# Kernel tuning notes

Measured on AMD Instinct MI355X. Metric: run time of the kernel, lower is better.

## Reference

```python
import jax, jax.numpy as jnp
import numpy as np

B, N, FIN, FOUT, H = 8, 2048, 128, 128, 2


def setup_inputs() -> dict:
    key = jax.random.key(0)
    k_h, k_adj, k_w, k_a = jax.random.split(key, 4)
    h = jax.random.normal(k_h, (B, N, FIN), dtype=jnp.float32)
    adj = jax.random.randint(k_adj, (B, N, N), 0, 2).astype(jnp.int32)
    # self-loops so no softmax row is all -inf
    idx = jnp.arange(N)
    adj = adj.at[:, idx, idx].set(1)
    W = jax.random.normal(k_w, (H, FIN, FOUT), dtype=jnp.float32) * 0.1
    a = jax.random.normal(k_a, (H, 2 * FOUT), dtype=jnp.float32) * 0.1
    return {"h": h, "adj": adj, "W": W, "a": a}


def reference(h, adj, W, a):
    # h: [B,N,FIN], adj: [B,N,N] int, W: [H,FIN,FOUT], a: [H,2*FOUT]
    Fout = W.shape[-1]
    Wh = jnp.einsum('bnf,hfo->bhno', h, W)              # [B,H,N,FOUT]
    # decompose a^T [Wh_i || Wh_j] = a1.Wh_i + a2.Wh_j (exact same math,
    # avoids the [B,N,N,2F] concat the torch code materializes)
    a1, a2 = a[:, :Fout], a[:, Fout:]
    s_i = jnp.einsum('bhno,ho->bhn', Wh, a1)            # score from node i
    s_j = jnp.einsum('bhno,ho->bhn', Wh, a2)            # score from node j
    e = jax.nn.leaky_relu(s_i[:, :, :, None] + s_j[:, :, None, :], 0.2)  # [B,H,N,N]
    e = jnp.where(adj[:, None, :, :] == 0, -jnp.inf, e)
    att = jax.nn.softmax(e, axis=-1)                    # [B,H,N,N]
    out = jnp.einsum('bhnm,bhmo->bhno', att, Wh)        # [B,H,N,FOUT]
    b, hh, n, f = out.shape
    # concat heads along feature dim (head order matches torch cat)
    return out.transpose(0, 2, 1, 3).reshape(b, n, hh * f)
```

## Files before the change

kernel.cpp:

```cpp
#include <hip/hip_runtime.h>
#include <math.h>

constexpr int Bv   = 8;
constexpr int Nv   = 2048;
constexpr int FIN  = 128;
constexpr int FOUT = 128;
constexpr int NH   = 2;
constexpr float LOG2E = 1.44269504088896340736f;

typedef __attribute__((ext_vector_type(8)))  short short8;
typedef __attribute__((ext_vector_type(4)))  float f32x4;
typedef __attribute__((ext_vector_type(16))) float f32x16;
typedef __attribute__((ext_vector_type(4)))  int   i32x4;
typedef unsigned long long u64;

static __device__ __forceinline__ unsigned short f2bf(float f) {
    unsigned u = __builtin_bit_cast(unsigned, f);
    u += 0x7fffu + ((u >> 16) & 1u);
    return (unsigned short)(u >> 16);
}
static __device__ __forceinline__ float bf2f(unsigned short s) {
    unsigned u = ((unsigned)s) << 16;
    return __builtin_bit_cast(float, u);
}
static __device__ __forceinline__ float fast_exp2(float x) {
#if __has_builtin(__builtin_amdgcn_exp2f)
    return __builtin_amdgcn_exp2f(x);
#else
    return exp2f(x);
#endif
}
static __device__ __forceinline__ unsigned cvt_pk_bf16(float lo, float hi) {
    unsigned r;
    asm("v_cvt_pk_bf16_f32 %0, %1, %2" : "=v"(r) : "v"(lo), "v"(hi));
    return r;
}

__global__ __launch_bounds__(256) void wa_kernel(const float* __restrict__ W,
                                                 const float* __restrict__ a,
                                                 float* __restrict__ wa,
                                                 unsigned short* __restrict__ wthi,
                                                 unsigned short* __restrict__ wtlo) {
    __shared__ unsigned short shi[FIN * 132];
    __shared__ unsigned short slo[FIN * 132];
    int hh = blockIdx.x;
    int t = threadIdx.x;

    const float* Ws = W + (size_t)hh * FIN * FOUT;
    for (int idx = t; idx < FIN * FOUT; idx += 256) {
        int f = idx >> 7, o = idx & 127;
        float wv = Ws[idx];
        unsigned short uh = f2bf(wv);
        shi[o * 132 + f] = uh;
        slo[o * 132 + f] = f2bf(wv - bf2f(uh));
    }

    int f = t >> 1, half = t & 1;
    const float* Wr = Ws + (size_t)f * FOUT + half * 64;
    const float* ar = a + (size_t)hh * 2 * FOUT + half * 64;
    float s1 = 0.f, s2 = 0.f;
    for (int o = 0; o < 64; o += 4) {
        float4 w4 = *(const float4*)&Wr[o];
        s1 += w4.x * ar[o] + w4.y * ar[o + 1] + w4.z * ar[o + 2] + w4.w * ar[o + 3];
        s2 += w4.x * ar[FOUT + o] + w4.y * ar[FOUT + o + 1] + w4.z * ar[FOUT + o + 2] + w4.w * ar[FOUT + o + 3];
    }
    s1 += __shfl_xor(s1, 1, 64);
    s2 += __shfl_xor(s2, 1, 64);
    if (half == 0) {
        wa[(hh * 2 + 0) * FIN + f] = s1 * LOG2E;
        wa[(hh * 2 + 1) * FIN + f] = s2 * LOG2E;
    }

    __syncthreads();
    unsigned short* dhi = wthi + (size_t)hh * FOUT * FIN;
    unsigned short* dlo = wtlo + (size_t)hh * FOUT * FIN;
    for (int idx = t; idx < FIN * FOUT; idx += 256) {
        int o = idx >> 7, ff = idx & 127;
        dhi[idx] = shi[o * 132 + ff];
        dlo[idx] = slo[o * 132 + ff];
    }
}

__global__ __launch_bounds__(256, 4) void prep_kernel(
    const float* __restrict__ h, const int* __restrict__ adj,
    const float* __restrict__ wa,
    const unsigned short* __restrict__ wthi, const unsigned short* __restrict__ wtlo,
    u64* __restrict__ adjp, unsigned short* __restrict__ whf,
    float* __restrict__ si, float* __restrict__ sj) {
    int bid = blockIdx.x;
    int t   = threadIdx.x;

    if (bid < 4096) {
        int wid = bid * 4 + (t >> 6);
        int l   = t & 63;
        int b   = wid >> 11;
        int r5  = wid & 2047;
        int jt  = r5 >> 6;
        int rb  = r5 & 63;
        const int* src = adj + ((size_t)b * Nv + rb * 32) * Nv + jt * 64 + l;
        u64* dst = adjp + ((size_t)b * 32 + jt) * Nv + rb * 32;
        for (int r = 0; r < 32; r += 8) {
            int av[8];
#pragma unroll
            for (int k = 0; k < 8; ++k) av[k] = src[(size_t)(r + k) * Nv];
            u64 m[8];
#pragma unroll
            for (int k = 0; k < 8; ++k) m[k] = __ballot(av[k] != 0);
            if (l == 0) {
#pragma unroll
                for (int k = 0; k < 8; k += 2) {
                    uint4 q = {(unsigned)m[k], (unsigned)(m[k] >> 32),
                               (unsigned)m[k + 1], (unsigned)(m[k + 1] >> 32)};
                    *(uint4*)&dst[r + k] = q;
                }
            }
        }
    } else if (bid < 8192) {
        int row  = (bid - 4096) * 4 + (t >> 6);
        int lane = t & 63;
        float x0 = h[(size_t)row * FIN + lane];
        float x1 = h[(size_t)row * FIN + 64 + lane];
        float s[4];
#pragma unroll
        for (int q = 0; q < 4; ++q) {
            const float* wp = wa + q * FIN;
            s[q] = x0 * wp[lane] + x1 * wp[64 + lane];
        }
#pragma unroll
        for (int m = 32; m >= 1; m >>= 1) {
#pragma unroll
            for (int q = 0; q < 4; ++q) s[q] += __shfl_xor(s[q], m, 64);
        }
        if (lane == 0) {
            int bb = row >> 11, n = row & (Nv - 1);
            si[((size_t)(bb * NH + 0)) * Nv + n] = s[0];
            sj[((size_t)(bb * NH + 0)) * Nv + n] = s[1];
            si[((size_t)(bb * NH + 1)) * Nv + n] = s[2];
            sj[((size_t)(bb * NH + 1)) * Nv + n] = s[3];
        }
    } else {
        int wb2 = bid - 8192;
        int bb  = wb2 & 7;
        int r2  = wb2 >> 3;
        int hh  = r2 & 1;
        int jtb = r2 >> 1;
        int n0  = jtb * 64;

        int w = t >> 6, l = t & 63, lo16 = l & 15, grp = l >> 4;
        int o0 = w * 32;

        const unsigned short* Whi = wthi + (size_t)hh * FOUT * FIN;
        const unsigned short* Wlo = wtlo + (size_t)hh * FOUT * FIN;
        short8 ahi[2][4], alo[2][4];
#pragma unroll
        for (int ot = 0; ot < 2; ++ot)
#pragma unroll
            for (int kt = 0; kt < 4; ++kt) {
                int off = (o0 + ot * 16 + lo16) * FIN + kt * 32 + grp * 8;
                ahi[ot][kt] = *(const short8*)&Whi[off];
                alo[ot][kt] = *(const short8*)&Wlo[off];
            }

        f32x4 acc[2][4];
#pragma unroll
        for (int ot = 0; ot < 2; ++ot)
#pragma unroll
            for (int nt = 0; nt < 4; ++nt) acc[ot][nt] = (f32x4){0.f, 0.f, 0.f, 0.f};

        const float* hb = h + ((size_t)bb * Nv + n0) * FIN;
#pragma unroll
        for (int nt = 0; nt < 4; ++nt) {
#pragma unroll
            for (int kt = 0; kt < 4; ++kt) {
                const float* hp = hb + (size_t)(nt * 16 + lo16) * FIN + kt * 32 + grp * 8;
                float4 x0 = *(const float4*)hp;
                float4 x1 = *(const float4*)(hp + 4);
                float xs[8] = {x0.x, x0.y, x0.z, x0.w, x1.x, x1.y, x1.z, x1.w};
                short8 bhi, blo;
#pragma unroll
                for (int i = 0; i < 8; ++i) {
                    unsigned short uh = f2bf(xs[i]);
                    bhi[i] = (short)uh;
                    blo[i] = (short)f2bf(xs[i] - bf2f(uh));
                }
#pragma unroll
                for (int ot = 0; ot < 2; ++ot) {
                    acc[ot][nt] = __builtin_amdgcn_mfma_f32_16x16x32_bf16(ahi[ot][kt], bhi, acc[ot][nt], 0, 0, 0);
                    acc[ot][nt] = __builtin_amdgcn_mfma_f32_16x16x32_bf16(ahi[ot][kt], blo, acc[ot][nt], 0, 0, 0);
                    acc[ot][nt] = __builtin_amdgcn_mfma_f32_16x16x32_bf16(alo[ot][kt], bhi, acc[ot][nt], 0, 0, 0);
                }
            }
        }
        unsigned short* db = whf + (size_t)(bb * NH + hh) * 262144;
#pragma unroll
        for (int ot = 0; ot < 2; ++ot)
#pragma unroll
            for (int nt = 0; nt < 4; ++nt)
#pragma unroll
                for (int reg = 0; reg < 4; ++reg) {
                    int oc = ot * 16 + grp * 4 + reg;
                    db[(size_t)(((jtb * 4 + nt) * 4 + w) * 64 + (lo16 >> 3) * 32 + oc) * 8 + (lo16 & 7)] =
                        f2bf(acc[ot][nt][reg]);
                }
    }
}

__global__ __launch_bounds__(256, 3) void gat_attn_kernel(
    const u64* __restrict__ adjp, const unsigned short* __restrict__ whf,
    const float* __restrict__ si, const float* __restrict__ sj,
    float* __restrict__ out) {
    int bid = blockIdx.x;
    int bb  = bid & 7;
    int r2  = bid >> 3;
    int rp  = r2 & 31;
    int hh  = (r2 >> 5) & 1;
    int ch  = r2 >> 6;

    int t = threadIdx.x, w = t >> 6, l = t & 63;
    int jp = w & 1, rw = w >> 1;
    int lo32 = l & 31, kh = l >> 5;
    int r0 = rp * 64 + rw * 32;
    int myrow = r0 + lo32;

    float sir = si[(size_t)(bb * NH + hh) * Nv + myrow];
    const u64*   adjr = adjp + (size_t)bb * 32 * Nv + myrow;
    const float* sjb  = sj + (size_t)(bb * NH + hh) * Nv;
    const unsigned short* wbp = whf + (size_t)(bb * NH + hh) * 262144 + (size_t)l * 8;

    f32x16 acc0, acc1, accL;
#pragma unroll
    for (int i = 0; i < 16; ++i) { acc0[i] = 0.f; acc1[i] = 0.f; accL[i] = 0.f; }

    const int ones_w = 0x3f803f80;
    short8 onesf = __builtin_bit_cast(short8, (i32x4){ones_w, ones_w, ones_w, ones_w});

    int jt0 = jp * 16;
    u64 mask = adjr[(size_t)jt0 * Nv];
    for (int jtl = 0; jtl < 16; ++jtl) {
        int jt = jt0 + jtl;
        int jb = jt * 64;
        const unsigned short* fb = wbp + (size_t)(jt * 16 + ch * 2) * 512;
        short8 bf[4][2];
#pragma unroll
        for (int kt = 0; kt < 4; ++kt) {
            bf[kt][0] = *(const short8*)(fb + (kt * 4 + 0) * 512);
            bf[kt][1] = *(const short8*)(fb + (kt * 4 + 1) * 512);
        }
        u64 mcur = mask;
        if (jtl < 15) mask = adjr[(size_t)(jt + 1) * Nv];

        short8 af[4];
#pragma unroll
        for (int kt = 0; kt < 4; ++kt) {
            unsigned mb = (unsigned)(mcur >> (kt * 16 + kh * 8)) & 0xFFu;
            const float* sp = &sjb[jb + kt * 16 + kh * 8];
            float4 s0 = *(const float4*)sp;
            float4 s1 = *(const float4*)(sp + 4);
            float x0 = sir + s0.x, x1 = sir + s0.y, x2 = sir + s0.z, x3 = sir + s0.w;
            float x4 = sir + s1.x, x5 = sir + s1.y, x6 = sir + s1.z, x7 = sir + s1.w;
            x0 = fmaxf(x0, 0.2f * x0); x1 = fmaxf(x1, 0.2f * x1);
            x2 = fmaxf(x2, 0.2f * x2); x3 = fmaxf(x3, 0.2f * x3);
            x4 = fmaxf(x4, 0.2f * x4); x5 = fmaxf(x5, 0.2f * x5);
            x6 = fmaxf(x6, 0.2f * x6); x7 = fmaxf(x7, 0.2f * x7);
            float p0 = fast_exp2(x0), p1 = fast_exp2(x1), p2 = fast_exp2(x2), p3 = fast_exp2(x3);
            float p4 = fast_exp2(x4), p5 = fast_exp2(x5), p6 = fast_exp2(x6), p7 = fast_exp2(x7);
            p0 = (mb & 1u)   ? p0 : 0.f;  p1 = (mb & 2u)   ? p1 : 0.f;
            p2 = (mb & 4u)   ? p2 : 0.f;  p3 = (mb & 8u)   ? p3 : 0.f;
            p4 = (mb & 16u)  ? p4 : 0.f;  p5 = (mb & 32u)  ? p5 : 0.f;
            p6 = (mb & 64u)  ? p6 : 0.f;  p7 = (mb & 128u) ? p7 : 0.f;
            unsigned w0 = cvt_pk_bf16(p0, p1), w1 = cvt_pk_bf16(p2, p3);
            unsigned w2 = cvt_pk_bf16(p4, p5), w3 = cvt_pk_bf16(p6, p7);
            af[kt] = __builtin_bit_cast(short8, (i32x4){(int)w0, (int)w1, (int)w2, (int)w3});
        }
#pragma unroll
        for (int kt = 0; kt < 4; ++kt) {
            acc0 = __builtin_amdgcn_mfma_f32_32x32x16_bf16(af[kt], bf[kt][0], acc0, 0, 0, 0);
            acc1 = __builtin_amdgcn_mfma_f32_32x32x16_bf16(af[kt], bf[kt][1], acc1, 0, 0, 0);
            accL = __builtin_amdgcn_mfma_f32_32x32x16_bf16(af[kt], onesf,    accL, 0, 0, 0);
        }
    }

    __shared__ float red[2][64][49];
    if (jp == 1) {
#pragma unroll
        for (int i = 0; i < 16; ++i) {
            red[rw][l][i]      = acc0[i];
            red[rw][l][16 + i] = acc1[i];
            red[rw][l][32 + i] = accL[i];
        }
    }
    __syncthreads();
    if (jp == 0) {
#pragma unroll
        for (int i = 0; i < 16; ++i) {
            acc0[i] += red[rw][l][i];
            acc1[i] += red[rw][l][16 + i];
            accL[i] += red[rw][l][32 + i];
        }
#pragma unroll
        for (int reg = 0; reg < 16; ++reg) {
            int rowc = (reg & 3) + 8 * (reg >> 2) + 4 * kh;
            float linv = 1.0f / accL[reg];
            float* op = out + ((size_t)(bb * Nv + r0 + rowc)) * (NH * FOUT) + hh * FOUT + ch * 64;
            op[lo32]      = acc0[reg] * linv;
            op[32 + lo32] = acc1[reg] * linv;
        }
    }
}

extern "C" void kernel_launch(void* const* d_in, const int* in_sizes, int n_in,
                              void* d_out, int out_size, void* d_ws, size_t ws_size,
                              hipStream_t stream) {
    const float* h   = (const float*)d_in[0];
    const int*   adj = (const int*)d_in[1];
    const float* W   = (const float*)d_in[2];
    const float* a   = (const float*)d_in[3];
    float*       out = (float*)d_out;

    char* ws = (char*)d_ws;
    unsigned short* whf  = (unsigned short*)ws;
    u64*            adjp = (u64*)(ws + 8388608);
    float* si = (float*)(ws + 8388608 + 4194304);
    float* sj = si + (size_t)Bv * NH * Nv;
    float* wa = sj + (size_t)Bv * NH * Nv;
    unsigned short* wthi = (unsigned short*)(wa + NH * 2 * FIN);
    unsigned short* wtlo = wthi + (size_t)NH * FOUT * FIN;

    wa_kernel  <<<dim3(2),    dim3(256), 0, stream>>>(W, a, wa, wthi, wtlo);
    prep_kernel<<<dim3(8704), dim3(256), 0, stream>>>(h, adj, wa, wthi, wtlo, adjp, whf, si, sj);
    gat_attn_kernel<<<dim3(1024), dim3(256), 0, stream>>>(adjp, whf, si, sj, out);
}
```

Before: 110.6 us.

## Pack adjacency bitmask row-wise with LDS transpose for coalesced stores

The adjacency bit-packing stage is restructured. Each block now handles 64 full rows of one batch, with each wave ballotting 16 rows across all 32 column tiles. The masks are staged in a shared-memory tile and then written to the packed layout with coalesced per-thread stores. This replaces single-lane uint4 stores and strided row reads. The block count drops from 4096 to 256, which may reduce the parallelism available to hide latency while reading the 134MB int adjacency matrix.

```diff
diff --git a/kernel.cpp b/kernel.cpp
--- a/kernel.cpp
+++ b/kernel.cpp
@@ -87,36 +87,42 @@
     const unsigned short* __restrict__ wthi, const unsigned short* __restrict__ wtlo,
     u64* __restrict__ adjp, unsigned short* __restrict__ whf,
     float* __restrict__ si, float* __restrict__ sj) {
+    __shared__ u64 plds[64][33];
+
     int bid = blockIdx.x;
     int t   = threadIdx.x;
 
-    if (bid < 4096) {
-        int wid = bid * 4 + (t >> 6);
-        int l   = t & 63;
-        int b   = wid >> 11;
-        int r5  = wid & 2047;
-        int jt  = r5 >> 6;
-        int rb  = r5 & 63;
-        const int* src = adj + ((size_t)b * Nv + rb * 32) * Nv + jt * 64 + l;
-        u64* dst = adjp + ((size_t)b * 32 + jt) * Nv + rb * 32;
-        for (int r = 0; r < 32; r += 8) {
-            int av[8];
-#pragma unroll
-            for (int k = 0; k < 8; ++k) av[k] = src[(size_t)(r + k) * Nv];
-            u64 m[8];
-#pragma unroll
-            for (int k = 0; k < 8; ++k) m[k] = __ballot(av[k] != 0);
-            if (l == 0) {
-#pragma unroll
-                for (int k = 0; k < 8; k += 2) {
-                    uint4 q = {(unsigned)m[k], (unsigned)(m[k] >> 32),
-                               (unsigned)m[k + 1], (unsigned)(m[k + 1] >> 32)};
-                    *(uint4*)&dst[r + k] = q;
+    if (bid < 256) {
+        int wv = t >> 6, l = t & 63;
+        int gb    = bid >> 5;
+        int rbase = (bid & 31) * 64 + wv * 16;
+        const int* src = adj + ((size_t)gb * Nv + rbase) * Nv + l;
+        for (int r = 0; r < 16; ++r) {
+            const int* rp = src + (size_t)r * Nv;
+#pragma unroll
+            for (int jt8 = 0; jt8 < 32; jt8 += 8) {
+                int av[8];
+#pragma unroll
+                for (int k = 0; k < 8; ++k) av[k] = rp[(jt8 + k) * 64];
+                u64 mm[8];
+#pragma unroll
+                for (int k = 0; k < 8; ++k) mm[k] = __ballot(av[k] != 0);
+                if (l == 0) {
+#pragma unroll
+                    for (int k = 0; k < 8; ++k) plds[wv * 16 + r][jt8 + k] = mm[k];
                 }
             }
         }
-    } else if (bid < 8192) {
-        int row  = (bid - 4096) * 4 + (t >> 6);
+        __syncthreads();
+        int n0B = (bid & 31) * 64;
+#pragma unroll
+        for (int i = 0; i < 8; ++i) {
+            int idx = i * 256 + t;
+            int jt = idx >> 6, row = idx & 63;
+            adjp[((size_t)gb * 32 + jt) * Nv + n0B + row] = plds[row][jt];
+        }
+    } else if (bid < 4352) {
+        int row  = (bid - 256) * 4 + (t >> 6);
         int lane = t & 63;
         float x0 = h[(size_t)row * FIN + lane];
         float x1 = h[(size_t)row * FIN + 64 + lane];
@@ -139,7 +145,7 @@
             sj[((size_t)(bb * NH + 1)) * Nv + n] = s[3];
         }
     } else {
-        int wb2 = bid - 8192;
+        int wb2 = bid - 4352;
         int bb  = wb2 & 7;
         int r2  = wb2 >> 3;
         int hh  = r2 & 1;
@@ -327,6 +333,6 @@
     unsigned short* wtlo = wthi + (size_t)NH * FOUT * FIN;
 
     wa_kernel  <<<dim3(2),    dim3(256), 0, stream>>>(W, a, wa, wthi, wtlo);
-    prep_kernel<<<dim3(8704), dim3(256), 0, stream>>>(h, adj, wa, wthi, wtlo, adjp, whf, si, sj);
+    prep_kernel<<<dim3(4864), dim3(256), 0, stream>>>(h, adj, wa, wthi, wtlo, adjp, whf, si, sj);
     gat_attn_kernel<<<dim3(1024), dim3(256), 0, stream>>>(adjp, whf, si, sj, out);
 }
```

Measured after the change: 106.1 us. 4.1% less time.
